# Performance work log

Hardware: AMD Instinct MI355X
Metric: run time of the kernel (lower is better)

The kernel has to match this reference:

```python
import jax, jax.numpy as jnp
import numpy as np

N = 50000      # points
K = 16         # neighbors per point
DIM = 256      # channels
H = 8          # heads
HD = DIM // H  # head dim


def setup_inputs() -> dict:
    key = jax.random.key(0)
    ks = jax.random.split(key, 8)
    feats = jax.random.normal(ks[0], (N, DIM), jnp.float32)
    xyz = jax.random.normal(ks[1], (N, 3), jnp.float32)
    # sorted segment ids: each point attends to exactly K neighbors
    index_0 = jnp.repeat(jnp.arange(N, dtype=jnp.int32), K)            # [M]
    index_1 = jax.random.randint(ks[2], (N * K,), 0, N, dtype=jnp.int32)  # [M]
    index_0_offsets = jnp.arange(N + 1, dtype=jnp.int32) * K
    s = 1.0 / np.sqrt(DIM)
    qkv_w = jax.random.normal(ks[3], (3 * DIM, DIM), jnp.float32) * s
    qkv_b = jax.random.normal(ks[4], (3 * DIM,), jnp.float32) * 0.01
    proj_w = jax.random.normal(ks[5], (DIM, DIM), jnp.float32) * s
    proj_b = jax.random.normal(ks[6], (DIM,), jnp.float32) * 0.01
    return {
        'feats': feats, 'xyz': xyz,
        'index_0': index_0, 'index_1': index_1,
        'index_0_offsets': index_0_offsets, 'n_max': K,
        'qkv_w': qkv_w, 'qkv_b': qkv_b, 'proj_w': proj_w, 'proj_b': proj_b,
    }


def reference(feats, xyz, index_0, index_1, index_0_offsets, n_max,
              qkv_w, qkv_b, proj_w, proj_b):
    n, c = feats.shape
    scale = (c // H) ** (-0.5)
    qkv = (feats @ qkv_w.T + qkv_b).reshape(n, 3, H, HD)  # [N,3,H,HD]
    q = qkv[:, 0] * scale
    k = qkv[:, 1]
    v = qkv[:, 2]
    # attention_step1: per-pair gathered dot product -> [M, H]
    attn = jnp.einsum('mhd,mhd->mh', q[index_0], k[index_1])
    # scatter_softmax over segments of index_0 (numerically stable)
    seg_max = jax.ops.segment_max(attn, index_0, num_segments=n)  # [N,H]
    e = jnp.exp(attn - seg_max[index_0])
    denom = jax.ops.segment_sum(e, index_0, num_segments=n)       # [N,H]
    attn = e / denom[index_0]                                     # [M,H]
    # attention_step2: scatter weighted sum of gathered values -> [N,H,HD]
    x = jax.ops.segment_sum(attn[:, :, None] * v[index_1], index_0,
                            num_segments=n)
    x = x.reshape(n, c)
    return x @ proj_w.T + proj_b
```

## Files before the change

kernel.cpp:

```cpp
#include <hip/hip_runtime.h>
#include <hip/hip_bf16.h>
#include <stdint.h>

typedef __bf16 bf16x8_t __attribute__((ext_vector_type(8)));
typedef float f32x4_t __attribute__((ext_vector_type(4)));

__device__ __forceinline__ float b2f(unsigned short u) {
    union { uint32_t i; float f; } x; x.i = ((uint32_t)u) << 16; return x.f;
}
__device__ __forceinline__ unsigned short f2b(float f) {
    union { float f; uint32_t i; } x; x.f = f;
    uint32_t r = (x.i + 0x7fffu + ((x.i >> 16) & 1u)) >> 16;
    return (unsigned short)r;
}
__device__ __forceinline__ void up2(uint32_t d, float& lo, float& hi) {
    union { uint32_t u; float f; } a, b;
    a.u = d << 16; b.u = d & 0xffff0000u;
    lo = a.f; hi = b.f;
}

#define QSCALE 0.17677669529663687f
#define NQ 50000

__global__ void prep_all(const float* __restrict__ feats, const float* __restrict__ qkv_w,
                         const float* __restrict__ proj_w, const float* __restrict__ qkv_b,
                         unsigned short* __restrict__ featsb, unsigned short* __restrict__ qkvwb,
                         unsigned short* __restrict__ projwb, float* __restrict__ qkvbS) {
    const int idx = blockIdx.x * 256 + threadIdx.x;
    const int NF = NQ * 256 / 4;
    if (idx < NF) {
        const int e = idx * 4;
        const float4 v = *reinterpret_cast<const float4*>(feats + e);
        ushort4 o;
        o.x = f2b(v.x); o.y = f2b(v.y); o.z = f2b(v.z); o.w = f2b(v.w);
        *reinterpret_cast<ushort4*>(featsb + e) = o;
    } else if (idx < NF + 49152) {
        const int e = (idx - NF) * 4;
        const float4 v = *reinterpret_cast<const float4*>(qkv_w + e);
        const float sc = (e >> 8) < 256 ? QSCALE : 1.f;
        ushort4 o;
        o.x = f2b(v.x * sc); o.y = f2b(v.y * sc); o.z = f2b(v.z * sc); o.w = f2b(v.w * sc);
        *reinterpret_cast<ushort4*>(qkvwb + e) = o;
    } else if (idx < NF + 49152 + 16384) {
        const int e = (idx - NF - 49152) * 4;
        const float4 v = *reinterpret_cast<const float4*>(proj_w + e);
        ushort4 o;
        o.x = f2b(v.x); o.y = f2b(v.y); o.z = f2b(v.z); o.w = f2b(v.w);
        *reinterpret_cast<ushort4*>(projwb + e) = o;
    } else if (idx < NF + 49152 + 16384 + 192) {
        const int e = (idx - NF - 49152 - 16384) * 4;
        float4 v = *reinterpret_cast<const float4*>(qkv_b + e);
        if (e < 256) { v.x *= QSCALE; v.y *= QSCALE; v.z *= QSCALE; v.w *= QSCALE; }
        *reinterpret_cast<float4*>(qkvbS + e) = v;
    }
}

template <int OUT_MODE, bool A_HM>
__launch_bounds__(256, 2)
__global__ void gemm_bf16(const unsigned short* __restrict__ A,
                          const unsigned short* __restrict__ W,
                          const float* __restrict__ bias,
                          void* __restrict__ Cout,
                          int M, int Nn, int Kk) {
    const int nCol = Nn >> 7;
    const int p = blockIdx.x;
    const int xcd = p & 7;
    const int q = p >> 3;
    const int c = q % nCol;
    const int rr = q / nCol;
    const int r = rr * 8 + xcd;
    const int blockRow = r * 128;
    if (blockRow >= M) return;
    const int blockCol = c * 128;

    __shared__ unsigned short As[128 * 64];
    __shared__ unsigned short Bs[128 * 64];
    const int t = threadIdx.x;
    const int w = t >> 6;
    const int l = t & 63;
    const int wm = w >> 1, wn = w & 1;

    f32x4_t acc[4][4];
#pragma unroll
    for (int i = 0; i < 4; ++i)
#pragma unroll
        for (int j = 0; j < 4; ++j) acc[i][j] = (f32x4_t)0.f;

    const int srow = t >> 3;
    const int scol = (((t & 7) ^ ((t >> 3) & 7)) * 8);

    for (int k0 = 0; k0 < Kk; k0 += 64) {
#pragma unroll
        for (int cc = 0; cc < 4; ++cc) {
            int arow = blockRow + cc * 32 + srow;
            arow = arow < M ? arow : M - 1;
            const int ak = k0 + scol;
            const unsigned short* ga = A_HM
                ? A + (size_t)(ak >> 5) * M * 32 + (size_t)arow * 32 + (ak & 31)
                : A + (size_t)arow * Kk + ak;
            const int brow = blockCol + cc * 32 + srow;
            const unsigned short* gb = W + (size_t)brow * Kk + k0 + scol;
            unsigned short* la = &As[cc * 2048 + w * 512];
            unsigned short* lb = &Bs[cc * 2048 + w * 512];
            __builtin_amdgcn_global_load_lds((const __attribute__((address_space(1))) void*)ga,
                                             (__attribute__((address_space(3))) void*)la, 16, 0, 0);
            __builtin_amdgcn_global_load_lds((const __attribute__((address_space(1))) void*)gb,
                                             (__attribute__((address_space(3))) void*)lb, 16, 0, 0);
        }
        __syncthreads();
        const int l15 = l & 15;
        const int lk = l >> 4;
        const int key = l & 7;
#pragma unroll
        for (int kc = 0; kc < 2; ++kc) {
            bf16x8_t af[4], bfr[4];
            const int cb = kc * 4 + lk;
            const int kof = (cb ^ key) * 8;
#pragma unroll
            for (int i = 0; i < 4; ++i) {
                af[i]  = *reinterpret_cast<const bf16x8_t*>(&As[(wm * 64 + i * 16 + l15) * 64 + kof]);
                bfr[i] = *reinterpret_cast<const bf16x8_t*>(&Bs[(wn * 64 + i * 16 + l15) * 64 + kof]);
            }
#pragma unroll
            for (int i = 0; i < 4; ++i)
#pragma unroll
                for (int j = 0; j < 4; ++j)
                    acc[i][j] = __builtin_amdgcn_mfma_f32_16x16x32_bf16(af[i], bfr[j], acc[i][j], 0, 0, 0);
        }
        __syncthreads();
    }

    const int lr = (l >> 4) * 4;
    const int lc = l & 15;
#pragma unroll
    for (int i = 0; i < 4; ++i) {
#pragma unroll
        for (int j = 0; j < 4; ++j) {
            const int col = blockCol + wn * 64 + j * 16 + lc;
            const float bz = bias[col];
#pragma unroll
            for (int rg = 0; rg < 4; ++rg) {
                const int row = blockRow + wm * 64 + i * 16 + lr + rg;
                if (row < M) {
                    const float val = acc[i][j][rg] + bz;
                    if (OUT_MODE == 0) {
                        ((float*)Cout)[(size_t)row * Nn + col] = val;
                    } else {
                        const int sec = col >> 8;
                        const int h = (col >> 5) & 7;
                        const int d = col & 31;
                        ((unsigned short*)Cout)[(size_t)sec * M * 256 + (size_t)h * M * 32
                                                + (size_t)row * 32 + d] = f2b(val);
                    }
                }
            }
        }
    }
}

__launch_bounds__(256, 4)
__global__ void attn_logits3(const unsigned short* __restrict__ qh,
                             const unsigned short* __restrict__ kh,
                             const int* __restrict__ index_1,
                             unsigned short* __restrict__ wh) {
    const int h = blockIdx.x & 7;
    const int slice = blockIdx.x >> 3;
    const int w = threadIdx.x >> 6;
    const int l = threadIdx.x & 63;
    const int g = l >> 3;
    const int p = l & 7;
    int i = slice * 32 + w * 8 + g;
    const bool valid = i < NQ;
    if (!valid) i = 0;

    const int4* ip = reinterpret_cast<const int4*>(index_1 + (size_t)i * 16);
    const int4 n0 = ip[0], n1 = ip[1], n2 = ip[2], n3 = ip[3];
    const int nbr[16] = { n0.x, n0.y, n0.z, n0.w, n1.x, n1.y, n1.z, n1.w,
                          n2.x, n2.y, n2.z, n2.w, n3.x, n3.y, n3.z, n3.w };

    const unsigned short* qhb = qh + (size_t)h * NQ * 32;
    const unsigned short* khb = kh + (size_t)h * NQ * 32;

    const ushort4 qu = *reinterpret_cast<const ushort4*>(qhb + (size_t)i * 32 + p * 4);
    const float qx = b2f(qu.x), qy = b2f(qu.y), qz = b2f(qu.z), qw = b2f(qu.w);

    float s[16];
#pragma unroll
    for (int m = 0; m < 16; ++m) {
        const ushort4 ku = *reinterpret_cast<const ushort4*>(khb + (size_t)nbr[m] * 32 + p * 4);
        float pv = qx * b2f(ku.x) + qy * b2f(ku.y) + qz * b2f(ku.z) + qw * b2f(ku.w);
        pv += __shfl_xor(pv, 1, 8);
        pv += __shfl_xor(pv, 2, 8);
        pv += __shfl_xor(pv, 4, 8);
        s[m] = pv;
    }
    float mx = s[0];
#pragma unroll
    for (int m = 1; m < 16; ++m) mx = fmaxf(mx, s[m]);
    float sum = 0.f;
#pragma unroll
    for (int m = 0; m < 16; ++m) { s[m] = __expf(s[m] - mx); sum += s[m]; }
    const float inv = 1.f / sum;

    if (valid) {
        const uint32_t pack = (uint32_t)f2b(s[2 * p] * inv) | ((uint32_t)f2b(s[2 * p + 1] * inv) << 16);
        ((uint32_t*)wh)[(size_t)h * NQ * 8 + (size_t)i * 8 + p] = pack;
    }
}

__launch_bounds__(256, 4)
__global__ void attn_out3(const unsigned short* __restrict__ vh,
                          const unsigned short* __restrict__ wh,
                          const int* __restrict__ index_1,
                          unsigned short* __restrict__ xh) {
    const int h = blockIdx.x & 7;
    const int slice = blockIdx.x >> 3;
    const int w = threadIdx.x >> 6;
    const int l = threadIdx.x & 63;
    const int g = l >> 3;
    const int p = l & 7;
    int i = slice * 32 + w * 8 + g;
    const bool valid = i < NQ;
    if (!valid) i = 0;

    const int4* ip = reinterpret_cast<const int4*>(index_1 + (size_t)i * 16);
    const int4 n0 = ip[0], n1 = ip[1], n2 = ip[2], n3 = ip[3];
    const int nbr[16] = { n0.x, n0.y, n0.z, n0.w, n1.x, n1.y, n1.z, n1.w,
                          n2.x, n2.y, n2.z, n2.w, n3.x, n3.y, n3.z, n3.w };

    const uint32_t* whp = (const uint32_t*)wh + (size_t)h * NQ * 8 + (size_t)i * 8;
    const uint4 w0 = *reinterpret_cast<const uint4*>(whp);
    const uint4 w1 = *reinterpret_cast<const uint4*>(whp + 4);
    const uint32_t wd[8] = { w0.x, w0.y, w0.z, w0.w, w1.x, w1.y, w1.z, w1.w };
    float wt[16];
#pragma unroll
    for (int j = 0; j < 8; ++j) up2(wd[j], wt[2 * j], wt[2 * j + 1]);

    const unsigned short* vhb = vh + (size_t)h * NQ * 32;
    float ax = 0.f, ay = 0.f, az = 0.f, aw = 0.f;
#pragma unroll
    for (int m = 0; m < 16; ++m) {
        const ushort4 vu = *reinterpret_cast<const ushort4*>(vhb + (size_t)nbr[m] * 32 + p * 4);
        ax += wt[m] * b2f(vu.x); ay += wt[m] * b2f(vu.y);
        az += wt[m] * b2f(vu.z); aw += wt[m] * b2f(vu.w);
    }
    if (valid) {
        ushort4 o;
        o.x = f2b(ax); o.y = f2b(ay); o.z = f2b(az); o.w = f2b(aw);
        *reinterpret_cast<ushort4*>(xh + (size_t)h * NQ * 32 + (size_t)i * 32 + p * 4) = o;
    }
}

extern "C" void kernel_launch(void* const* d_in, const int* in_sizes, int n_in,
                              void* d_out, int out_size, void* d_ws, size_t ws_size,
                              hipStream_t stream) {
    const float* feats   = (const float*)d_in[0];
    const int*   index_1 = (const int*)d_in[3];
    const float* qkv_w   = (const float*)d_in[6];
    const float* qkv_b   = (const float*)d_in[7];
    const float* proj_w  = (const float*)d_in[8];
    const float* proj_b  = (const float*)d_in[9];
    float* out = (float*)d_out;

    const int N = NQ, DIM = 256, QKVD = 768;

    unsigned short* featsb = (unsigned short*)d_ws;
    unsigned short* qkvwb  = featsb + (size_t)N * DIM;
    unsigned short* projwb = qkvwb + (size_t)QKVD * DIM;
    float*          qkvbS  = (float*)(projwb + (size_t)DIM * DIM);
    unsigned short* qkvh   = (unsigned short*)(qkvbS + QKVD);
    unsigned short* qh     = qkvh;
    unsigned short* kh     = qkvh + (size_t)N * DIM;
    unsigned short* vh     = qkvh + (size_t)2 * N * DIM;
    unsigned short* xh     = qkvh + (size_t)3 * N * DIM;
    unsigned short* wh     = xh + (size_t)N * DIM;

    const int prepQuads = N * 256 / 4 + 49152 + 16384 + 192;
    prep_all<<<(prepQuads + 255) / 256, 256, 0, stream>>>(
        feats, qkv_w, proj_w, qkv_b, featsb, qkvwb, projwb, qkvbS);

    const int nRow = (N + 127) / 128;
    const int nRowPad = ((nRow + 7) / 8) * 8;
    const int attnBlocks = ((N + 31) / 32) * 8;

    gemm_bf16<1, false><<<nRowPad * (QKVD / 128), 256, 0, stream>>>(featsb, qkvwb, qkvbS, qkvh, N, QKVD, DIM);
    attn_logits3<<<attnBlocks, 256, 0, stream>>>(qh, kh, index_1, wh);
    attn_out3<<<attnBlocks, 256, 0, stream>>>(vh, wh, index_1, xh);
    gemm_bf16<0, true><<<nRowPad * (DIM / 128), 256, 0, stream>>>(xh, projwb, proj_b, out, N, DIM, DIM);
}
```

Before: 272.4 us.

## Compute attention logits with bf16 MFMA over gathered key tiles

Replaces the shuffle-reduced scalar dot-product logits kernel with one where each wave handles 16 queries. For each query it gathers the 16 neighbour key rows as an MFMA 16x16x32 A fragment against a fragment of 16 queries, keeping only the matching column. Softmax over the 16 neighbours now uses cross-lane shuffles over the accumulator rows. Key gathers become 16-byte loads and the per-lane dot-product ALU work plus shuffles go away. In exchange most of the MFMA output is discarded, and the logits kernel gets its own grid size.

```diff
diff --git a/kernel.cpp b/kernel.cpp
--- a/kernel.cpp
+++ b/kernel.cpp
@@ -147,9 +147,9 @@
                         ((float*)Cout)[(size_t)row * Nn + col] = val;
                     } else {
                         const int sec = col >> 8;
-                        const int h = (col >> 5) & 7;
+                        const int hh = (col >> 5) & 7;
                         const int d = col & 31;
-                        ((unsigned short*)Cout)[(size_t)sec * M * 256 + (size_t)h * M * 32
+                        ((unsigned short*)Cout)[(size_t)sec * M * 256 + (size_t)hh * M * 32
                                                 + (size_t)row * 32 + d] = f2b(val);
                     }
                 }
@@ -159,7 +159,7 @@
 }
 
 __launch_bounds__(256, 4)
-__global__ void attn_logits3(const unsigned short* __restrict__ qh,
+__global__ void attn_logits4(const unsigned short* __restrict__ qh,
                              const unsigned short* __restrict__ kh,
                              const int* __restrict__ index_1,
                              unsigned short* __restrict__ wh) {
@@ -167,44 +167,49 @@
     const int slice = blockIdx.x >> 3;
     const int w = threadIdx.x >> 6;
     const int l = threadIdx.x & 63;
-    const int g = l >> 3;
-    const int p = l & 7;
-    int i = slice * 32 + w * 8 + g;
-    const bool valid = i < NQ;
-    if (!valid) i = 0;
-
-    const int4* ip = reinterpret_cast<const int4*>(index_1 + (size_t)i * 16);
-    const int4 n0 = ip[0], n1 = ip[1], n2 = ip[2], n3 = ip[3];
-    const int nbr[16] = { n0.x, n0.y, n0.z, n0.w, n1.x, n1.y, n1.z, n1.w,
-                          n2.x, n2.y, n2.z, n2.w, n3.x, n3.y, n3.z, n3.w };
+    const int col = l & 15;
+    const int krow = l >> 4;
+    const int qbase = slice * 64 + w * 16;
 
     const unsigned short* qhb = qh + (size_t)h * NQ * 32;
     const unsigned short* khb = kh + (size_t)h * NQ * 32;
 
-    const ushort4 qu = *reinterpret_cast<const ushort4*>(qhb + (size_t)i * 32 + p * 4);
-    const float qx = b2f(qu.x), qy = b2f(qu.y), qz = b2f(qu.z), qw = b2f(qu.w);
-
-    float s[16];
-#pragma unroll
-    for (int m = 0; m < 16; ++m) {
-        const ushort4 ku = *reinterpret_cast<const ushort4*>(khb + (size_t)nbr[m] * 32 + p * 4);
-        float pv = qx * b2f(ku.x) + qy * b2f(ku.y) + qz * b2f(ku.z) + qw * b2f(ku.w);
-        pv += __shfl_xor(pv, 1, 8);
-        pv += __shfl_xor(pv, 2, 8);
-        pv += __shfl_xor(pv, 4, 8);
-        s[m] = pv;
-    }
-    float mx = s[0];
-#pragma unroll
-    for (int m = 1; m < 16; ++m) mx = fmaxf(mx, s[m]);
-    float sum = 0.f;
-#pragma unroll
-    for (int m = 0; m < 16; ++m) { s[m] = __expf(s[m] - mx); sum += s[m]; }
-    const float inv = 1.f / sum;
-
-    if (valid) {
-        const uint32_t pack = (uint32_t)f2b(s[2 * p] * inv) | ((uint32_t)f2b(s[2 * p + 1] * inv) << 16);
-        ((uint32_t*)wh)[(size_t)h * NQ * 8 + (size_t)i * 8 + p] = pack;
+    int qcol = qbase + col; qcol = qcol < NQ ? qcol : NQ - 1;
+    const bf16x8_t bfrag = *reinterpret_cast<const bf16x8_t*>(qhb + (size_t)qcol * 32 + krow * 8);
+
+    int idx[16];
+#pragma unroll
+    for (int j = 0; j < 16; ++j) {
+        int qj = qbase + j; qj = qj < NQ ? qj : NQ - 1;
+        idx[j] = index_1[(size_t)qj * 16 + col];
+    }
+
+    float s0 = 0.f, s1 = 0.f, s2 = 0.f, s3 = 0.f;
+#pragma unroll
+    for (int j = 0; j < 16; ++j) {
+        const bf16x8_t afrag = *reinterpret_cast<const bf16x8_t*>(khb + (size_t)idx[j] * 32 + krow * 8);
+        const f32x4_t d = __builtin_amdgcn_mfma_f32_16x16x32_bf16(afrag, bfrag, (f32x4_t)0.f, 0, 0, 0);
+        const bool mine = (col == j);
+        s0 = mine ? d[0] : s0;
+        s1 = mine ? d[1] : s1;
+        s2 = mine ? d[2] : s2;
+        s3 = mine ? d[3] : s3;
+    }
+
+    float mx = fmaxf(fmaxf(s0, s1), fmaxf(s2, s3));
+    mx = fmaxf(mx, __shfl_xor(mx, 16, 64));
+    mx = fmaxf(mx, __shfl_xor(mx, 32, 64));
+    float e0 = __expf(s0 - mx), e1 = __expf(s1 - mx), e2 = __expf(s2 - mx), e3 = __expf(s3 - mx);
+    float sm = e0 + e1 + e2 + e3;
+    sm += __shfl_xor(sm, 16, 64);
+    sm += __shfl_xor(sm, 32, 64);
+    const float inv = 1.f / sm;
+
+    if (qbase + col < NQ) {
+        const uint32_t d0 = (uint32_t)f2b(e0 * inv) | ((uint32_t)f2b(e1 * inv) << 16);
+        const uint32_t d1 = (uint32_t)f2b(e2 * inv) | ((uint32_t)f2b(e3 * inv) << 16);
+        *reinterpret_cast<uint2*>(wh + (size_t)h * NQ * 16 + (size_t)(qbase + col) * 16 + krow * 4)
+            = make_uint2(d0, d1);
     }
 }
 
@@ -281,10 +286,11 @@
 
     const int nRow = (N + 127) / 128;
     const int nRowPad = ((nRow + 7) / 8) * 8;
-    const int attnBlocks = ((N + 31) / 32) * 8;
+    const int logitsBlocks = ((N + 63) / 64) * 8;
+    const int outBlocks    = ((N + 31) / 32) * 8;
 
     gemm_bf16<1, false><<<nRowPad * (QKVD / 128), 256, 0, stream>>>(featsb, qkvwb, qkvbS, qkvh, N, QKVD, DIM);
-    attn_logits3<<<attnBlocks, 256, 0, stream>>>(qh, kh, index_1, wh);
-    attn_out3<<<attnBlocks, 256, 0, stream>>>(vh, wh, index_1, xh);
+    attn_logits4<<<logitsBlocks, 256, 0, stream>>>(qh, kh, index_1, wh);
+    attn_out3<<<outBlocks, 256, 0, stream>>>(vh, wh, index_1, xh);
     gemm_bf16<0, true><<<nRowPad * (DIM / 128), 256, 0, stream>>>(xh, projwb, proj_b, out, N, DIM, DIM);
 }
```

Result: no change. 268.0 us (-1.6%).
